# Optimization experiments

Measured on AMD Instinct MI355X. Metric: run time of the kernel, lower is better.

Reference implementation:

```python
import jax, jax.numpy as jnp
import numpy as np

B, S, D, G, N_ORIG = 4, 4096, 512, 64, 4096
EPS_NORM = 1e-12   # F.normalize eps
EPS_MERGE = 1e-8   # merge-weight eps


def setup_inputs() -> dict:
    key = jax.random.key(0)
    k1, k2, k3 = jax.random.split(key, 3)
    x = jax.random.normal(k1, (B, S, D), dtype=jnp.float32)
    source = jax.random.uniform(k2, (B, S, N_ORIG), dtype=jnp.float32)
    position_ids = jnp.arange(B * S, dtype=jnp.int64).reshape(B, S)
    W = jax.random.normal(k3, (D, G), dtype=jnp.float32) * 0.05  # group_proj weight (no bias)
    return {"x": x, "source": source, "position_ids": position_ids,
            "r": 1024, "window_size": 16, "W": W}


def _token_merge(x, source, position_ids, r, window_size, W):
    Bb, Ss, Dd = x.shape
    r = min(r, Ss // 2)
    idx = jnp.arange(Ss, dtype=jnp.int32)
    # local candidate pairs: |i-j| = d for d in 1..window_size-1
    pi = jnp.concatenate([idx[:Ss - d] for d in range(1, min(window_size, Ss))])
    pj = jnp.concatenate([idx[d:] for d in range(1, min(window_size, Ss))])

    g = x @ W                                   # (B,S,G)
    norms = jnp.linalg.norm(g, axis=-1)         # (B,S)
    gn = g / jnp.maximum(norms, EPS_NORM)[..., None]
    sim = jnp.einsum('bpg,bpg->bp', gn[:, pi], gn[:, pj])  # (B,P)

    def greedy(sim_b):
        # deterministic order: score DESC, i ASC, j ASC
        order = jnp.lexsort((pj, pi, -sim_b))
        oi, oj = pi[order], pj[order]

        def step(carry, ij):
            used, partner, cnt = carry
            i, j = ij
            take = (cnt < r) & (~used[i]) & (~used[j])
            used = used.at[i].set(used[i] | take).at[j].set(used[j] | take)
            partner = partner.at[i].set(jnp.where(take, j, partner[i]))
            cnt = cnt + take.astype(jnp.int32)
            return (used, partner, cnt), None

        init = (jnp.zeros(Ss, bool), jnp.full(Ss, -1, jnp.int32), jnp.int32(0))
        (used, partner, cnt), _ = jax.lax.scan(step, init, (oi, oj))
        return partner  # partner[i] = j if pair (i,j) selected, else -1

    partner = jax.vmap(greedy)(sim)  # (B,S)

    def merge(xb, sb, pb, partner_b, norms_b):
        sel = partner_b >= 0
        pj_safe = jnp.where(sel, partner_b, idx)
        wi = norms_b
        wj = jnp.where(sel, norms_b[pj_safe], 0.0)
        merged = (wi[:, None] * xb + wj[:, None] * xb[pj_safe]) / (wi + wj + EPS_MERGE)[:, None]
        x_m = jnp.where(sel[:, None], merged, xb)
        s_m = sb + jnp.where(sel, 1.0, 0.0)[:, None] * sb[pj_safe]
        # drop the second token of each merged pair, preserving order
        skip_idx = jnp.where(sel, partner_b, Ss)
        skip = jnp.zeros(Ss, bool).at[skip_idx].set(True, mode='drop')
        keep = jnp.argsort(skip.astype(jnp.int8), stable=True)[: Ss - r]
        return x_m[keep], s_m[keep], pb[keep]

    return jax.vmap(merge)(x, source, position_ids, partner, norms)


def reference(x, source, position_ids, r, window_size, W):
    return _token_merge(x, source, position_ids, r, window_size, W)
```

## Files before the change

### kernel.cpp

```cpp
#include <hip/hip_runtime.h>

#define BATCH 4
#define SLEN 4096
#define DDIM 512
#define GDIM 64
#define NORIG 4096
#define WMAX 15
#define RSEL 1024
#define KEEP (SLEN - RSEL)
#define NTOK (BATCH * SLEN)
#define PEEL_ROUNDS 256

#define OFF_TCODE ((size_t)0)
#define OFF_TCNT  ((size_t)16384)
#define OFF_LISTS ((size_t)32768)
#define OFF_GN    ((size_t)0)
#define OFF_SIMST ((size_t)8388608)
#define OFF_NORMS ((size_t)10485760)
#define OFF_KT    ((size_t)10584064)
#define OFF_PJR   ((size_t)10633216)
#define OFF_WIR   ((size_t)10682368)
#define OFF_WJR   ((size_t)10731520)
#define WS_NEEDED ((size_t)10780672)

#define OUTX_OFF 0
#define OUTS_OFF 6291456
#define OUTP_OFF 56623104

__global__ __launch_bounds__(256) void k_proj(const float* __restrict__ x,
                                              const float* __restrict__ Wm,
                                              double* __restrict__ gn,
                                              float* __restrict__ norms) {
  __shared__ float xs[16 * DDIM];
  int base = blockIdx.x * 16;
  const float4* src = (const float4*)(x + (size_t)base * DDIM);
  float4* dstv = (float4*)xs;
  for (int idx = threadIdx.x; idx < 16 * DDIM / 4; idx += 256) dstv[idx] = src[idx];
  __syncthreads();
  int lane = threadIdx.x & 63;
  int wv = threadIdx.x >> 6;
  double acc0 = 0, acc1 = 0, acc2 = 0, acc3 = 0;
  const float* xw = xs + wv * 4 * DDIM;
  for (int d = 0; d < DDIM; ++d) {
    double wval = (double)Wm[d * GDIM + lane];
    acc0 += (double)xw[d] * wval;
    acc1 += (double)xw[DDIM + d] * wval;
    acc2 += (double)xw[2 * DDIM + d] * wval;
    acc3 += (double)xw[3 * DDIM + d] * wval;
  }
  double accs[4] = {acc0, acc1, acc2, acc3};
  for (int k = 0; k < 4; ++k) {
    double a = accs[k];
    double ss = a * a;
    for (int o = 32; o >= 1; o >>= 1) ss += __shfl_xor(ss, o, 64);
    double nrm = sqrt(ss);
    int tok = base + wv * 4 + k;
    if (lane == 0) norms[tok] = (float)nrm;
    double denom = nrm > 1e-12 ? nrm : 1e-12;
    gn[(size_t)tok * GDIM + lane] = a / denom;
  }
}

__global__ __launch_bounds__(256) void k_sims(const double* __restrict__ gn,
                                              double* __restrict__ simsT) {
  int blk = blockIdx.x;
  int b = blk >> 6;
  int t0 = (blk & 63) * 64;
  int nrows = min(64 + WMAX, SLEN - t0);
  __shared__ double gs[(64 + WMAX) * GDIM];
  const double* src = gn + ((size_t)b * SLEN + t0) * GDIM;
  for (int idx = threadIdx.x; idx < nrows * GDIM; idx += 256) gs[idx] = src[idx];
  __syncthreads();
  int lane = threadIdx.x & 63, wv = threadIdx.x >> 6;
  for (int s = wv; s < 64 * WMAX; s += 4) {
    int il = s & 63, d = (s >> 6) + 1;
    int i = t0 + il;
    if (i + d < SLEN) {
      double p = gs[il * GDIM + lane] * gs[(il + d) * GDIM + lane];
      for (int o = 32; o >= 1; o >>= 1) p += __shfl_xor(p, o, 64);
      if (lane == 0) simsT[((size_t)(b * SLEN + i)) * 16 + d] = p;
    }
  }
}

__global__ __launch_bounds__(256) void k_lists(const double* __restrict__ simsT,
                                               unsigned short* __restrict__ lists) {
  __shared__ unsigned short stage[4][32];
  int wave = threadIdx.x >> 6, lane = threadIdx.x & 63;
  int t = blockIdx.x * 4 + wave;
  int b = t >> 12, tt = t & (SLEN - 1);
  const double* sb = simsT + (size_t)b * SLEN * 16;
  int d = (lane >> 1) + 1;
  int side = lane & 1;
  bool valid = (lane < 30) && (side == 0 ? (tt + d < SLEN) : (tt - d >= 0));
  unsigned long long key = 0ULL;
  unsigned int code = 0xFFFFu;
  if (valid) {
    int i = (side == 0) ? tt : (tt - d);
    double s = sb[(size_t)i * 16 + d];
    unsigned long long bits = (unsigned long long)__double_as_longlong(s);
    key = (bits & 0x8000000000000000ULL) ? ~bits : (bits | 0x8000000000000000ULL);
    code = (unsigned int)((i << 4) | d);
  }
  int rank = 0;
#pragma clang loop unroll(disable)
  for (int q = 0; q < 30; ++q) {
    unsigned long long kq = __shfl(key, q, 64);
    unsigned int cq = __shfl(code, q, 64);
    if (kq != 0ULL && (kq > key || (kq == key && cq < code))) rank++;
  }
  if (lane < 32) stage[wave][lane] = 0xFFFFu;
  if (valid) stage[wave][rank] = (unsigned short)code;
  if (lane < 32) lists[(size_t)t * 32 + lane] = stage[wave][lane];
}

__global__ __launch_bounds__(1024) void k_peel(const unsigned short* __restrict__ lists,
                                               unsigned short* __restrict__ tcodeG,
                                               int* __restrict__ tcntG) {
  int b = blockIdx.x;
  const unsigned short* lb = lists + (size_t)b * SLEN * 32;
  __shared__ unsigned short bestPair[SLEN];
  __shared__ unsigned char used[SLEN];
  __shared__ unsigned char cur[SLEN];
  __shared__ unsigned short takenCode[2048];
  __shared__ int takenCnt, baseCnt;
  int tid = threadIdx.x;
#pragma clang loop unroll(disable)
  for (int t = tid; t < SLEN; t += 1024) {
    used[t] = 0; cur[t] = 0;
    bestPair[t] = lb[(size_t)t * 32];
  }
  if (tid == 0) takenCnt = 0;
  __syncthreads();

#pragma clang loop unroll(disable)
  for (int round = 0; round < PEEL_ROUNDS; ++round) {
    if (tid == 0) baseCnt = takenCnt;
    __syncthreads();
#pragma clang loop unroll(disable)
    for (int t = tid; t < SLEN; t += 1024) {
      unsigned short c = bestPair[t];
      if (c != 0xFFFFu && (c >> 4) == t && !used[t]) {
        int j = t + (c & 15);
        if (bestPair[j] == c && !used[j]) {
          int idx = atomicAdd(&takenCnt, 1);
          if (idx < 2048) takenCode[idx] = c;
          used[t] = 1; used[j] = 1;
        }
      }
    }
    __syncthreads();
    int newCnt = takenCnt;
    if (newCnt == baseCnt) break;
#pragma clang loop unroll(disable)
    for (int t = tid; t < SLEN; t += 1024) {
      if (used[t]) { bestPair[t] = 0xFFFFu; continue; }
      unsigned short c = bestPair[t];
      if (c == 0xFFFFu) continue;
      int i = c >> 4, d = c & 15;
      int p = (i == t) ? (t + d) : i;
      int cc = cur[t];
#pragma clang loop unroll(disable)
      while (c != 0xFFFFu && used[p]) {
        ++cc;
        c = (cc < 32) ? lb[(size_t)t * 32 + cc] : (unsigned short)0xFFFFu;
        if (c != 0xFFFFu) { i = c >> 4; d = c & 15; p = (i == t) ? (t + d) : i; }
      }
      cur[t] = (unsigned char)cc;
      bestPair[t] = c;
    }
    __syncthreads();
  }

  int m = min(takenCnt, 2048);
#pragma clang loop unroll(disable)
  for (int k = tid; k < m; k += 1024) tcodeG[b * 2048 + k] = takenCode[k];
  if (tid == 0) tcntG[b] = m;
}

__global__ __launch_bounds__(1024) void k_rank(const double* __restrict__ simsT_all,
                                               const unsigned short* __restrict__ tcodeG,
                                               const int* __restrict__ tcntG,
                                               const float* __restrict__ norms,
                                               int* __restrict__ kt, int* __restrict__ pjr,
                                               float* __restrict__ wir, float* __restrict__ wjr,
                                               float* __restrict__ out_pos) {
  int b = blockIdx.x;
  const double* simsT = simsT_all + (size_t)b * SLEN * 16;
  __shared__ unsigned long long key[2048];
  __shared__ unsigned short code[2048];
  __shared__ unsigned char state[2048];
  __shared__ unsigned int hist[256];
  __shared__ unsigned int bcum[256];
  __shared__ unsigned int wsum[4];
  __shared__ int sharedB, sharedNeed, sdone, allAccept;
  __shared__ unsigned short memberIdx[2048];
  __shared__ int memberCnt;
  __shared__ unsigned char skipA[SLEN];
  __shared__ unsigned char mergeD[SLEN];
  __shared__ int wTot[16], wOff[16];
  int tid = threadIdx.x;
  int m = min(tcntG[b], 2048);
#pragma clang loop unroll(disable)
  for (int t = tid; t < SLEN; t += 1024) { skipA[t] = 0; mergeD[t] = 0; }
#pragma clang loop unroll(disable)
  for (int k = tid; k < m; k += 1024) {
    unsigned short c = tcodeG[b * 2048 + k];
    code[k] = c;
    state[k] = 0;
    double s = simsT[(size_t)(c >> 4) * 16 + (c & 15)];
    unsigned long long bits = (unsigned long long)__double_as_longlong(s);
    key[k] = (bits & 0x8000000000000000ULL) ? ~bits : (bits | 0x8000000000000000ULL);
  }
  if (tid == 0) { sharedNeed = RSEL; sdone = 0; allAccept = (m <= RSEL); memberCnt = 0; }
  __syncthreads();

  if (!allAccept) {
#pragma clang loop unroll(disable)
    for (int pass = 0; pass < 8; ++pass) {
      if (tid < 256) hist[tid] = 0;
      __syncthreads();
      int sh = 56 - 8 * pass;
#pragma clang loop unroll(disable)
      for (int k = tid; k < m; k += 1024)
        if (!state[k]) atomicAdd(&hist[(unsigned int)(key[k] >> sh) & 0xFFu], 1u);
      __syncthreads();
      unsigned int v = 0, inc = 0;
      int lane = tid & 63, w = tid >> 6;
      if (tid < 256) {
        v = hist[255 - tid];
        inc = v;
        for (int o = 1; o < 64; o <<= 1) { unsigned int n = __shfl_up(inc, o, 64); if (lane >= o) inc += n; }
        if (lane == 63) wsum[w] = inc;
      }
      __syncthreads();
      if (tid < 256) {
        unsigned int off = 0;
        for (int ww = 0; ww < w; ++ww) off += wsum[ww];
        unsigned int incl = inc + off;
        bcum[255 - tid] = incl - v;
      }
      __syncthreads();
      if (tid < 256) {
        int bkt = 255 - tid;
        unsigned int ag = bcum[bkt];
        unsigned int need = (unsigned int)sharedNeed;
        if (ag < need && ag + hist[bkt] >= need) sharedB = bkt;
      }
      __syncthreads();
      int B = sharedB;
      unsigned int needInB = (unsigned int)sharedNeed - bcum[B];
#pragma clang loop unroll(disable)
      for (int k = tid; k < m; k += 1024) {
        if (!state[k]) {
          unsigned int bv = (unsigned int)(key[k] >> sh) & 0xFFu;
          if ((int)bv > B) state[k] = 1;
          else if ((int)bv < B) state[k] = 2;
        }
      }
      __syncthreads();
      if (tid == 0) {
        sharedNeed = (int)needInB;
        if (hist[B] == needInB) sdone = 1;
      }
      __syncthreads();
      if (sdone) break;
    }
  }
  __syncthreads();

  if (allAccept || sdone) {
#pragma clang loop unroll(disable)
    for (int k = tid; k < m; k += 1024) if (!state[k]) state[k] = 1;
  } else {
#pragma clang loop unroll(disable)
    for (int k = tid; k < m; k += 1024)
      if (!state[k]) { int idx = atomicAdd(&memberCnt, 1); memberIdx[idx] = (unsigned short)k; }
    __syncthreads();
    int mc = memberCnt;
    unsigned int need = (unsigned int)sharedNeed;
#pragma clang loop unroll(disable)
    for (int z = tid; z < mc; z += 1024) {
      int k = memberIdx[z];
      unsigned short ck = code[k];
      unsigned int wr = 0;
#pragma clang loop unroll(disable)
      for (int q2 = 0; q2 < mc; ++q2) if (code[memberIdx[q2]] < ck) wr++;
      if (wr < need) state[k] = 1;
    }
  }
  __syncthreads();
#pragma clang loop unroll(disable)
  for (int k = tid; k < m; k += 1024) {
    if (state[k] == 1) {
      unsigned short ck = code[k];
      int i = ck >> 4, d = ck & 15;
      mergeD[i] = (unsigned char)d;
      skipA[i + d] = 1;
    }
  }
  __syncthreads();
  int cnt = 0; unsigned char kf[4];
  int tbase = tid * 4;
  for (int u = 0; u < 4; ++u) { kf[u] = skipA[tbase + u] ? 0 : 1; cnt += kf[u]; }
  int lane = tid & 63, wv = tid >> 6;
  int incl = cnt;
  for (int o = 1; o < 64; o <<= 1) { int n = __shfl_up(incl, o, 64); if (lane >= o) incl += n; }
  if (lane == 63) wTot[wv] = incl;
  __syncthreads();
  if (tid < 16) {
    int v2 = wTot[tid];
    for (int o = 1; o < 16; o <<= 1) { int n = __shfl_up(v2, o, 64); if (lane >= o) v2 += n; }
    wOff[tid] = v2 - wTot[tid];
  }
  __syncthreads();
  int pos = wOff[wv] + (incl - cnt);
  for (int u = 0; u < 4; ++u) {
    int t = tbase + u;
    if (kf[u]) {
      if (pos < KEEP) {
        int orow = b * KEEP + pos;
        kt[orow] = t;
        int d = mergeD[t];
        pjr[orow] = d ? (t + d) : -1;
        wir[orow] = norms[b * SLEN + t];
        wjr[orow] = d ? norms[b * SLEN + t + d] : 0.0f;
        out_pos[orow] = (float)(b * SLEN + t);
      }
      pos++;
    }
  }
}

__global__ __launch_bounds__(128) void k_gather_x(const float* __restrict__ x,
                                                  const int* __restrict__ kt, const int* __restrict__ pjr,
                                                  const float* __restrict__ wir, const float* __restrict__ wjr,
                                                  float* __restrict__ outx) {
  int orow = blockIdx.x;
  int b = orow / KEEP;
  int t = kt[orow], pj = pjr[orow];
  int gi = min(max(b * SLEN + t, 0), NTOK - 1);
  const float4* xi = (const float4*)(x + (size_t)gi * DDIM);
  float4* o = (float4*)(outx + (size_t)orow * DDIM);
  int c = threadIdx.x;
  float4 v = xi[c];
  if (pj >= 0) {
    int gj = min(b * SLEN + min(pj, SLEN - 1), NTOK - 1);
    const float4* xj = (const float4*)(x + (size_t)gj * DDIM);
    float4 u = xj[c];
    float wi = wir[orow], wj = wjr[orow];
    float inv = 1.0f / (wi + wj + 1e-8f);
    v.x = (wi * v.x + wj * u.x) * inv;
    v.y = (wi * v.y + wj * u.y) * inv;
    v.z = (wi * v.z + wj * u.z) * inv;
    v.w = (wi * v.w + wj * u.w) * inv;
  }
  o[c] = v;
}

__global__ __launch_bounds__(256) void k_gather_s(const float* __restrict__ src,
                                                  const int* __restrict__ kt, const int* __restrict__ pjr,
                                                  float* __restrict__ outs) {
  int orow = blockIdx.x;
  int b = orow / KEEP;
  int t = kt[orow], pj = pjr[orow];
  int gi = min(max(b * SLEN + t, 0), NTOK - 1);
  const float4* si = (const float4*)(src + (size_t)gi * NORIG);
  float4* o = (float4*)(outs + (size_t)orow * NORIG);
  if (pj >= 0) {
    int gj = min(b * SLEN + min(pj, SLEN - 1), NTOK - 1);
    const float4* sj = (const float4*)(src + (size_t)gj * NORIG);
    for (int u = 0; u < 4; ++u) {
      int c = threadIdx.x + u * 256;
      float4 a = si[c], bb = sj[c];
      a.x += bb.x; a.y += bb.y; a.z += bb.z; a.w += bb.w;
      o[c] = a;
    }
  } else {
    for (int u = 0; u < 4; ++u) { int c = threadIdx.x + u * 256; o[c] = si[c]; }
  }
}

extern "C" void kernel_launch(void* const* d_in, const int* in_sizes, int n_in,
                              void* d_out, int out_size, void* d_ws, size_t ws_size,
                              hipStream_t stream) {
  if (ws_size < WS_NEEDED) return;

  const float* x = (const float*)d_in[0];
  const float* source = (const float*)d_in[1];
  const float* Wm = (const float*)d_in[5];

  char* ws = (char*)d_ws;
  double* gn = (double*)(ws + OFF_GN);
  double* simsT = (double*)(ws + OFF_SIMST);
  float* norms = (float*)(ws + OFF_NORMS);
  unsigned short* tcode = (unsigned short*)(ws + OFF_TCODE);
  int* tcnt = (int*)(ws + OFF_TCNT);
  unsigned short* lists = (unsigned short*)(ws + OFF_LISTS);
  int* kt = (int*)(ws + OFF_KT);
  int* pjr = (int*)(ws + OFF_PJR);
  float* wir = (float*)(ws + OFF_WIR);
  float* wjr = (float*)(ws + OFF_WJR);

  float* out = (float*)d_out;
  float* outx = out + OUTX_OFF;
  float* outs = out + OUTS_OFF;
  float* outp = out + OUTP_OFF;

  k_proj<<<(BATCH * SLEN) / 16, 256, 0, stream>>>(x, Wm, gn, norms);
  k_sims<<<BATCH * (SLEN / 64), 256, 0, stream>>>(gn, simsT);
  k_lists<<<NTOK / 4, 256, 0, stream>>>(simsT, lists);
  k_peel<<<BATCH, 1024, 0, stream>>>(lists, tcode, tcnt);
  k_rank<<<BATCH, 1024, 0, stream>>>(simsT, tcode, tcnt, norms, kt, pjr, wir, wjr, outp);
  k_gather_x<<<BATCH * KEEP, 128, 0, stream>>>(x, kt, pjr, wir, wjr, outx);
  k_gather_s<<<BATCH * KEEP, 256, 0, stream>>>(source, kt, pjr, outs);
}
```

Baseline: 364.8 us.

## Fuse peel and rank kernels, compact preference lists to byte deltas in LDS

```diff
diff --git a/kernel.cpp b/kernel.cpp
--- a/kernel.cpp
+++ b/kernel.cpp
@@ -10,10 +10,9 @@
 #define KEEP (SLEN - RSEL)
 #define NTOK (BATCH * SLEN)
 #define PEEL_ROUNDS 256
-
-#define OFF_TCODE ((size_t)0)
-#define OFF_TCNT  ((size_t)16384)
-#define OFF_LISTS ((size_t)32768)
+#define LDSL 8
+
+#define OFF_LISTS ((size_t)0)
 #define OFF_GN    ((size_t)0)
 #define OFF_SIMST ((size_t)8388608)
 #define OFF_NORMS ((size_t)10485760)
@@ -84,8 +83,8 @@
 }
 
 __global__ __launch_bounds__(256) void k_lists(const double* __restrict__ simsT,
-                                               unsigned short* __restrict__ lists) {
-  __shared__ unsigned short stage[4][32];
+                                               signed char* __restrict__ lists8) {
+  __shared__ signed char stage[4][32];
   int wave = threadIdx.x >> 6, lane = threadIdx.x & 63;
   int t = blockIdx.x * 4 + wave;
   int b = t >> 12, tt = t & (SLEN - 1);
@@ -95,12 +94,14 @@
   bool valid = (lane < 30) && (side == 0 ? (tt + d < SLEN) : (tt - d >= 0));
   unsigned long long key = 0ULL;
   unsigned int code = 0xFFFFu;
+  signed char delta = 0;
   if (valid) {
     int i = (side == 0) ? tt : (tt - d);
     double s = sb[(size_t)i * 16 + d];
     unsigned long long bits = (unsigned long long)__double_as_longlong(s);
     key = (bits & 0x8000000000000000ULL) ? ~bits : (bits | 0x8000000000000000ULL);
     code = (unsigned int)((i << 4) | d);
+    delta = (side == 0) ? (signed char)d : (signed char)(-d);
   }
   int rank = 0;
 #pragma clang loop unroll(disable)
@@ -109,26 +110,39 @@
     unsigned int cq = __shfl(code, q, 64);
     if (kq != 0ULL && (kq > key || (kq == key && cq < code))) rank++;
   }
-  if (lane < 32) stage[wave][lane] = 0xFFFFu;
-  if (valid) stage[wave][rank] = (unsigned short)code;
-  if (lane < 32) lists[(size_t)t * 32 + lane] = stage[wave][lane];
-}
-
-__global__ __launch_bounds__(1024) void k_peel(const unsigned short* __restrict__ lists,
-                                               unsigned short* __restrict__ tcodeG,
-                                               int* __restrict__ tcntG) {
+  if (lane < 32) stage[wave][lane] = 0;
+  if (valid) stage[wave][rank] = delta;
+  if (lane < 32) lists8[(size_t)t * 32 + lane] = stage[wave][lane];
+}
+
+__global__ __launch_bounds__(1024) void k_match(const signed char* __restrict__ lists8,
+                                                const double* __restrict__ simsT_all,
+                                                const float* __restrict__ norms,
+                                                int* __restrict__ kt, int* __restrict__ pjr,
+                                                float* __restrict__ wir, float* __restrict__ wjr,
+                                                float* __restrict__ out_pos) {
   int b = blockIdx.x;
-  const unsigned short* lb = lists + (size_t)b * SLEN * 32;
-  __shared__ unsigned short bestPair[SLEN];
+  const signed char* lb = lists8 + (size_t)b * SLEN * 32;
+  const double* simsT = simsT_all + (size_t)b * SLEN * 16;
+  __shared__ __align__(16) unsigned char big[32768];
+  __shared__ signed char bp[SLEN];
   __shared__ unsigned char used[SLEN];
   __shared__ unsigned char cur[SLEN];
   __shared__ unsigned short takenCode[2048];
+  __shared__ unsigned char meta[SLEN];
   __shared__ int takenCnt, baseCnt;
+  __shared__ int sharedB, sharedNeed, sdone, allAccept;
+  __shared__ int memberCnt;
+  __shared__ int wTot[16], wOff[16];
+  signed char* l8 = (signed char*)big;
   int tid = threadIdx.x;
+
 #pragma clang loop unroll(disable)
   for (int t = tid; t < SLEN; t += 1024) {
-    used[t] = 0; cur[t] = 0;
-    bestPair[t] = lb[(size_t)t * 32];
+    unsigned long long v = *(const unsigned long long*)(lb + (size_t)t * 32);
+    *(unsigned long long*)(l8 + t * LDSL) = v;
+    bp[t] = (signed char)(v & 0xFF);
+    used[t] = 0; cur[t] = 0; meta[t] = 0;
   }
   if (tid == 0) takenCnt = 0;
   __syncthreads();
@@ -139,12 +153,12 @@
     __syncthreads();
 #pragma clang loop unroll(disable)
     for (int t = tid; t < SLEN; t += 1024) {
-      unsigned short c = bestPair[t];
-      if (c != 0xFFFFu && (c >> 4) == t && !used[t]) {
-        int j = t + (c & 15);
-        if (bestPair[j] == c && !used[j]) {
+      int dlt = bp[t];
+      if (dlt > 0 && !used[t]) {
+        int j = t + dlt;
+        if (!used[j] && bp[j] == (signed char)(-dlt)) {
           int idx = atomicAdd(&takenCnt, 1);
-          if (idx < 2048) takenCode[idx] = c;
+          if (idx < 2048) takenCode[idx] = (unsigned short)((t << 4) | dlt);
           used[t] = 1; used[j] = 1;
         }
       }
@@ -154,59 +168,37 @@
     if (newCnt == baseCnt) break;
 #pragma clang loop unroll(disable)
     for (int t = tid; t < SLEN; t += 1024) {
-      if (used[t]) { bestPair[t] = 0xFFFFu; continue; }
-      unsigned short c = bestPair[t];
-      if (c == 0xFFFFu) continue;
-      int i = c >> 4, d = c & 15;
-      int p = (i == t) ? (t + d) : i;
+      if (used[t]) { bp[t] = 0; continue; }
+      int dlt = bp[t];
+      if (dlt == 0) continue;
+      int p = t + dlt;
       int cc = cur[t];
 #pragma clang loop unroll(disable)
-      while (c != 0xFFFFu && used[p]) {
+      while (dlt != 0 && used[p]) {
         ++cc;
-        c = (cc < 32) ? lb[(size_t)t * 32 + cc] : (unsigned short)0xFFFFu;
-        if (c != 0xFFFFu) { i = c >> 4; d = c & 15; p = (i == t) ? (t + d) : i; }
+        dlt = (cc < LDSL) ? l8[t * LDSL + cc]
+            : ((cc < 32) ? lb[(size_t)t * 32 + cc] : (signed char)0);
+        p = t + dlt;
       }
       cur[t] = (unsigned char)cc;
-      bestPair[t] = c;
+      bp[t] = (signed char)dlt;
     }
     __syncthreads();
   }
 
+  unsigned long long* key = (unsigned long long*)big;
+  unsigned short* codeA = (unsigned short*)(big + 16384);
+  unsigned char* state = (unsigned char*)(big + 20480);
+  unsigned int* hist = (unsigned int*)(big + 22528);
+  unsigned int* bcum = (unsigned int*)(big + 23552);
+  unsigned int* wsum = (unsigned int*)(big + 24576);
+  unsigned short* memberIdx = (unsigned short*)(big + 24704);
   int m = min(takenCnt, 2048);
-#pragma clang loop unroll(disable)
-  for (int k = tid; k < m; k += 1024) tcodeG[b * 2048 + k] = takenCode[k];
-  if (tid == 0) tcntG[b] = m;
-}
-
-__global__ __launch_bounds__(1024) void k_rank(const double* __restrict__ simsT_all,
-                                               const unsigned short* __restrict__ tcodeG,
-                                               const int* __restrict__ tcntG,
-                                               const float* __restrict__ norms,
-                                               int* __restrict__ kt, int* __restrict__ pjr,
-                                               float* __restrict__ wir, float* __restrict__ wjr,
-                                               float* __restrict__ out_pos) {
-  int b = blockIdx.x;
-  const double* simsT = simsT_all + (size_t)b * SLEN * 16;
-  __shared__ unsigned long long key[2048];
-  __shared__ unsigned short code[2048];
-  __shared__ unsigned char state[2048];
-  __shared__ unsigned int hist[256];
-  __shared__ unsigned int bcum[256];
-  __shared__ unsigned int wsum[4];
-  __shared__ int sharedB, sharedNeed, sdone, allAccept;
-  __shared__ unsigned short memberIdx[2048];
-  __shared__ int memberCnt;
-  __shared__ unsigned char skipA[SLEN];
-  __shared__ unsigned char mergeD[SLEN];
-  __shared__ int wTot[16], wOff[16];
-  int tid = threadIdx.x;
-  int m = min(tcntG[b], 2048);
-#pragma clang loop unroll(disable)
-  for (int t = tid; t < SLEN; t += 1024) { skipA[t] = 0; mergeD[t] = 0; }
+  __syncthreads();
 #pragma clang loop unroll(disable)
   for (int k = tid; k < m; k += 1024) {
-    unsigned short c = tcodeG[b * 2048 + k];
-    code[k] = c;
+    unsigned short c = takenCode[k];
+    codeA[k] = c;
     state[k] = 0;
     double s = simsT[(size_t)(c >> 4) * 16 + (c & 15)];
     unsigned long long bits = (unsigned long long)__double_as_longlong(s);
@@ -282,10 +274,10 @@
 #pragma clang loop unroll(disable)
     for (int z = tid; z < mc; z += 1024) {
       int k = memberIdx[z];
-      unsigned short ck = code[k];
+      unsigned short ck = codeA[k];
       unsigned int wr = 0;
 #pragma clang loop unroll(disable)
-      for (int q2 = 0; q2 < mc; ++q2) if (code[memberIdx[q2]] < ck) wr++;
+      for (int q2 = 0; q2 < mc; ++q2) if (codeA[memberIdx[q2]] < ck) wr++;
       if (wr < need) state[k] = 1;
     }
   }
@@ -293,16 +285,16 @@
 #pragma clang loop unroll(disable)
   for (int k = tid; k < m; k += 1024) {
     if (state[k] == 1) {
-      unsigned short ck = code[k];
+      unsigned short ck = codeA[k];
       int i = ck >> 4, d = ck & 15;
-      mergeD[i] = (unsigned char)d;
-      skipA[i + d] = 1;
+      meta[i] = (unsigned char)d;
+      meta[i + d] = 0x80;
     }
   }
   __syncthreads();
   int cnt = 0; unsigned char kf[4];
   int tbase = tid * 4;
-  for (int u = 0; u < 4; ++u) { kf[u] = skipA[tbase + u] ? 0 : 1; cnt += kf[u]; }
+  for (int u = 0; u < 4; ++u) { kf[u] = (meta[tbase + u] & 0x80) ? 0 : 1; cnt += kf[u]; }
   int lane = tid & 63, wv = tid >> 6;
   int incl = cnt;
   for (int o = 1; o < 64; o <<= 1) { int n = __shfl_up(incl, o, 64); if (lane >= o) incl += n; }
@@ -321,7 +313,7 @@
       if (pos < KEEP) {
         int orow = b * KEEP + pos;
         kt[orow] = t;
-        int d = mergeD[t];
+        int d = meta[t] & 15;
         pjr[orow] = d ? (t + d) : -1;
         wir[orow] = norms[b * SLEN + t];
         wjr[orow] = d ? norms[b * SLEN + t + d] : 0.0f;
@@ -332,52 +324,44 @@
   }
 }
 
-__global__ __launch_bounds__(128) void k_gather_x(const float* __restrict__ x,
-                                                  const int* __restrict__ kt, const int* __restrict__ pjr,
-                                                  const float* __restrict__ wir, const float* __restrict__ wjr,
-                                                  float* __restrict__ outx) {
+__global__ __launch_bounds__(256) void k_gather(const float* __restrict__ x,
+                                                const float* __restrict__ src,
+                                                const int* __restrict__ kt, const int* __restrict__ pjr,
+                                                const float* __restrict__ wir, const float* __restrict__ wjr,
+                                                float* __restrict__ outx, float* __restrict__ outs) {
   int orow = blockIdx.x;
   int b = orow / KEEP;
   int t = kt[orow], pj = pjr[orow];
   int gi = min(max(b * SLEN + t, 0), NTOK - 1);
-  const float4* xi = (const float4*)(x + (size_t)gi * DDIM);
-  float4* o = (float4*)(outx + (size_t)orow * DDIM);
+  int gj = min(b * SLEN + min(max(pj, 0), SLEN - 1), NTOK - 1);
   int c = threadIdx.x;
-  float4 v = xi[c];
-  if (pj >= 0) {
-    int gj = min(b * SLEN + min(pj, SLEN - 1), NTOK - 1);
-    const float4* xj = (const float4*)(x + (size_t)gj * DDIM);
-    float4 u = xj[c];
-    float wi = wir[orow], wj = wjr[orow];
-    float inv = 1.0f / (wi + wj + 1e-8f);
-    v.x = (wi * v.x + wj * u.x) * inv;
-    v.y = (wi * v.y + wj * u.y) * inv;
-    v.z = (wi * v.z + wj * u.z) * inv;
-    v.w = (wi * v.w + wj * u.w) * inv;
-  }
-  o[c] = v;
-}
-
-__global__ __launch_bounds__(256) void k_gather_s(const float* __restrict__ src,
-                                                  const int* __restrict__ kt, const int* __restrict__ pjr,
-                                                  float* __restrict__ outs) {
-  int orow = blockIdx.x;
-  int b = orow / KEEP;
-  int t = kt[orow], pj = pjr[orow];
-  int gi = min(max(b * SLEN + t, 0), NTOK - 1);
+  if (c < 128) {
+    const float4* xi = (const float4*)(x + (size_t)gi * DDIM);
+    float4 v = xi[c];
+    if (pj >= 0) {
+      const float4* xj = (const float4*)(x + (size_t)gj * DDIM);
+      float4 u = xj[c];
+      float wi = wir[orow], wj = wjr[orow];
+      float inv = 1.0f / (wi + wj + 1e-8f);
+      v.x = (wi * v.x + wj * u.x) * inv;
+      v.y = (wi * v.y + wj * u.y) * inv;
+      v.z = (wi * v.z + wj * u.z) * inv;
+      v.w = (wi * v.w + wj * u.w) * inv;
+    }
+    ((float4*)(outx + (size_t)orow * DDIM))[c] = v;
+  }
   const float4* si = (const float4*)(src + (size_t)gi * NORIG);
   float4* o = (float4*)(outs + (size_t)orow * NORIG);
   if (pj >= 0) {
-    int gj = min(b * SLEN + min(pj, SLEN - 1), NTOK - 1);
     const float4* sj = (const float4*)(src + (size_t)gj * NORIG);
     for (int u = 0; u < 4; ++u) {
-      int c = threadIdx.x + u * 256;
-      float4 a = si[c], bb = sj[c];
+      int c2 = c + u * 256;
+      float4 a = si[c2], bb = sj[c2];
       a.x += bb.x; a.y += bb.y; a.z += bb.z; a.w += bb.w;
-      o[c] = a;
+      o[c2] = a;
     }
   } else {
-    for (int u = 0; u < 4; ++u) { int c = threadIdx.x + u * 256; o[c] = si[c]; }
+    for (int u = 0; u < 4; ++u) { int c2 = c + u * 256; o[c2] = si[c2]; }
   }
 }
 
@@ -394,9 +378,7 @@
   double* gn = (double*)(ws + OFF_GN);
   double* simsT = (double*)(ws + OFF_SIMST);
   float* norms = (float*)(ws + OFF_NORMS);
-  unsigned short* tcode = (unsigned short*)(ws + OFF_TCODE);
-  int* tcnt = (int*)(ws + OFF_TCNT);
-  unsigned short* lists = (unsigned short*)(ws + OFF_LISTS);
+  signed char* lists8 = (signed char*)(ws + OFF_LISTS);
   int* kt = (int*)(ws + OFF_KT);
   int* pjr = (int*)(ws + OFF_PJR);
   float* wir = (float*)(ws + OFF_WIR);
@@ -409,9 +391,7 @@
 
   k_proj<<<(BATCH * SLEN) / 16, 256, 0, stream>>>(x, Wm, gn, norms);
   k_sims<<<BATCH * (SLEN / 64), 256, 0, stream>>>(gn, simsT);
-  k_lists<<<NTOK / 4, 256, 0, stream>>>(simsT, lists);
-  k_peel<<<BATCH, 1024, 0, stream>>>(lists, tcode, tcnt);
-  k_rank<<<BATCH, 1024, 0, stream>>>(simsT, tcode, tcnt, norms, kt, pjr, wir, wjr, outp);
-  k_gather_x<<<BATCH * KEEP, 128, 0, stream>>>(x, kt, pjr, wir, wjr, outx);
-  k_gather_s<<<BATCH * KEEP, 256, 0, stream>>>(source, kt, pjr, outs);
-}
+  k_lists<<<NTOK / 4, 256, 0, stream>>>(simsT, lists8);
+  k_match<<<BATCH, 1024, 0, stream>>>(lists8, simsT, norms, kt, pjr, wir, wjr, outp);
+  k_gather<<<BATCH * KEEP, 256, 0, stream>>>(x, source, kt, pjr, wir, wjr, outx, outs);
+}
```

Measured after the change: 354.9 us. 1.03x faster.
